# Kernel tuning notes

Hardware: AMD Instinct MI355X
Metric: run time of the kernel (lower is better)

## Reference

```python
import jax, jax.numpy as jnp
import numpy as np

B, S, H, NCOL, NH = 32, 512, 768, 32, 12
HD = H // NH  # head dim 64
LN_EPS = 1e-12


def setup_inputs() -> dict:
    key = jax.random.key(0)
    ks = jax.random.split(key, 20)
    s = 0.02
    inp = {
        'hidden_states': jax.random.normal(ks[0], (B, S, H), jnp.float32),
        'column_embeddings': jax.random.normal(ks[1], (B, NCOL, H), jnp.float32),
        'column_categories': jax.random.randint(ks[2], (B, NCOL), 0, 2, jnp.int32),
        'value_mask': jax.random.randint(ks[3], (B, S), 0, NCOL + 1, jnp.int32),
        'Wd': jax.random.normal(ks[4], (H, H), jnp.float32) * s,
        'bd': jnp.zeros((H,), jnp.float32),
        'Wc': jax.random.normal(ks[5], (H, H), jnp.float32) * s,
        'bc': jnp.zeros((H,), jnp.float32),
        'Wq': jax.random.normal(ks[6], (H, H), jnp.float32) * s,
        'bq': jnp.zeros((H,), jnp.float32),
        'Wk': jax.random.normal(ks[7], (H, H), jnp.float32) * s,
        'bk': jnp.zeros((H,), jnp.float32),
        'Wv': jax.random.normal(ks[8], (H, H), jnp.float32) * s,
        'bv': jnp.zeros((H,), jnp.float32),
        'Wo': jax.random.normal(ks[9], (H, H), jnp.float32) * s,
        'bo': jnp.zeros((H,), jnp.float32),
        'ln_g': jnp.ones((H,), jnp.float32),
        'ln_b': jnp.zeros((H,), jnp.float32),
    }
    return inp


def _layernorm(x, g, b):
    mu = jnp.mean(x, axis=-1, keepdims=True)
    var = jnp.mean(jnp.square(x - mu), axis=-1, keepdims=True)
    return (x - mu) * jax.lax.rsqrt(var + LN_EPS) * g + b


def reference(hidden_states, column_embeddings, column_categories, value_mask,
              Wd, bd, Wc, bc, Wq, bq, Wk, bk, Wv, bv, Wo, bo, ln_g, ln_b):
    # dense branch
    h_ = hidden_states @ Wd.T + bd  # [B,S,H]
    # column gather: zero out category==0 columns, prepend zero row for index 0
    table = column_embeddings * (column_categories == 1)[..., None].astype(column_embeddings.dtype)
    table = jnp.concatenate([jnp.zeros_like(table[:, :1]), table], axis=1)  # [B,NCOL+1,H]
    h_col = jnp.take_along_axis(table, value_mask[..., None].astype(jnp.int32), axis=1)  # [B,S,H]
    h = jax.nn.gelu(h_ + (h_col @ Wc.T + bc), approximate=False)
    # Roberta self-attention
    def heads(x):
        return x.reshape(B, S, NH, HD).transpose(0, 2, 1, 3)  # [B,NH,S,HD]
    q = heads(h @ Wq.T + bq)
    k = heads(h @ Wk.T + bk)
    v = heads(h @ Wv.T + bv)
    scores = jnp.einsum('bhsd,bhtd->bhst', q, k) / jnp.sqrt(jnp.float32(HD))
    probs = jax.nn.softmax(scores, axis=-1)
    ctx = jnp.einsum('bhst,bhtd->bhsd', probs, v).transpose(0, 2, 1, 3).reshape(B, S, H)
    # self-output: dense + residual + layernorm
    out = _layernorm(ctx @ Wo.T + bo + h, ln_g, ln_b)
    return out
```

## Files before the change

kernel.cpp:

```cpp
#include <hip/hip_runtime.h>
#include <hip/hip_bf16.h>
#include <math.h>
#include <stdint.h>

#define B_    32
#define S_    512
#define H_    768
#define NH_   12
#define HD_   64
#define NCOL_ 32
#define M_    (B_*S_)

typedef __bf16 bf16;
typedef __bf16 bf16x8 __attribute__((ext_vector_type(8)));
typedef __bf16 bf16x4 __attribute__((ext_vector_type(4)));
typedef float  f32x4  __attribute__((ext_vector_type(4)));

__device__ __forceinline__ void async_load16(const void* g, void* l) {
    __builtin_amdgcn_global_load_lds(
        (__attribute__((address_space(1))) unsigned int*)g,
        (__attribute__((address_space(3))) unsigned int*)l, 16, 0, 0);
}

__device__ __forceinline__ bf16x8 cvt8(const float* p) {
    const float4* fp = (const float4*)p;
    float4 x = fp[0], y = fp[1];
    bf16x8 r;
    r[0] = (bf16)x.x; r[1] = (bf16)x.y; r[2] = (bf16)x.z; r[3] = (bf16)x.w;
    r[4] = (bf16)y.x; r[5] = (bf16)y.y; r[6] = (bf16)y.z; r[7] = (bf16)y.w;
    return r;
}

__global__ __launch_bounds__(256) void cvt_kernel(
    const float* __restrict__ hidden, const float* __restrict__ ce,
    const int* __restrict__ cc, const int* __restrict__ vm,
    const float* __restrict__ Wd, const float* __restrict__ Wc,
    const float* __restrict__ Wq, const float* __restrict__ Wk,
    const float* __restrict__ Wv, const float* __restrict__ Wo,
    const float* __restrict__ bq, const float* __restrict__ bk,
    const float* __restrict__ bv,
    bf16* __restrict__ hbf, bf16* __restrict__ hcol,
    bf16* __restrict__ wpack, float* __restrict__ bqkv)
{
    int blk = blockIdx.x;
    if (blk < 6144) {
        int id = blk * 256 + threadIdx.x;
        int row = id / 96, c = id - row * 96;
        *(bf16x8*)&hbf[(long)row * H_ + c * 8] = cvt8(hidden + (long)row * H_ + c * 8);
    } else if (blk < 12288) {
        int id = (blk - 6144) * 256 + threadIdx.x;
        int row = id / 96, c = id - row * 96;
        int b = row >> 9;
        int m = vm[row];
        bf16x8 val;
#pragma unroll
        for (int i = 0; i < 8; i++) val[i] = (bf16)0.0f;
        if (m > 0) {
            int col = m - 1;
            if (cc[b * NCOL_ + col] == 1)
                val = cvt8(ce + ((long)(b * NCOL_ + col)) * H_ + c * 8);
        }
        *(bf16x8*)&hcol[(long)row * H_ + c * 8] = val;
    } else {
        int id = (blk - 12288) * 256 + threadIdx.x;
        if (id < 442368) {
            const float* src;
            int r = id;
            if      (r < 73728)  { src = Wd; }
            else if (r < 147456) { src = Wc; r -= 73728; }
            else if (r < 221184) { src = Wq; r -= 147456; }
            else if (r < 294912) { src = Wk; r -= 221184; }
            else if (r < 368640) { src = Wv; r -= 294912; }
            else                 { src = Wo; r -= 368640; }
            *(bf16x8*)&wpack[(long)id * 8] = cvt8(src + (long)r * 8);
        } else if (id < 442656) {
            int j0 = (id - 442368) * 8;
#pragma unroll
            for (int i = 0; i < 8; i++) {
                int j = j0 + i;
                float v = (j < 768) ? bq[j] : (j < 1536) ? bk[j - 768] : bv[j - 1536];
                bqkv[j] = v;
            }
        }
    }
}

template<int MODE>
__global__ __launch_bounds__(256, 3) void gemm_bt(
    const bf16* __restrict__ A0, const bf16* __restrict__ A1,
    const bf16* __restrict__ B0, const bf16* __restrict__ B1,
    const float* __restrict__ bias1, const float* __restrict__ bias2,
    const bf16* __restrict__ resid, bf16* __restrict__ out,
    int K, int KSPLIT)
{
    __shared__ __align__(16) bf16 SA[3][128 * 32];
    __shared__ __align__(16) bf16 SB[3][128 * 32];

    const int tid  = threadIdx.x;
    const int lane = tid & 63;
    const int wave = tid >> 6;
    const int wr   = wave >> 1;
    const int wc   = wave & 1;
    const int quad = lane >> 4;
    const int ln16 = lane & 15;
    const int m0   = blockIdx.x * 128;
    const int n0   = blockIdx.y * 128;

    int arow[2], acol[2];
#pragma unroll
    for (int q = 0; q < 2; q++) {
        int l = q * 256 + tid;
        int row = l >> 2;
        arow[q] = row;
        acol[q] = ((l & 3) ^ ((row >> 1) & 3)) * 8;
    }

    auto stage = [&](int kt, int bsel) {
        int kk = kt * 32;
        const bf16* ag = (kk < KSPLIT) ? A0 + kk : A1 + (kk - KSPLIT);
        const bf16* bg = (kk < KSPLIT) ? B0 + kk : B1 + (kk - KSPLIT);
        async_load16(ag + (long)(m0 + arow[0]) * H_ + acol[0], &SA[bsel][tid * 8]);
        async_load16(ag + (long)(m0 + arow[1]) * H_ + acol[1], &SA[bsel][2048 + tid * 8]);
        async_load16(bg + (long)(n0 + arow[0]) * H_ + acol[0], &SB[bsel][tid * 8]);
        async_load16(bg + (long)(n0 + arow[1]) * H_ + acol[1], &SB[bsel][2048 + tid * 8]);
    };

    f32x4 acc[4][4];
    const f32x4 zero4 = {0.f, 0.f, 0.f, 0.f};
#pragma unroll
    for (int i = 0; i < 4; i++)
#pragma unroll
        for (int j = 0; j < 4; j++) acc[i][j] = zero4;

    const int s4 = (ln16 >> 1) & 3;
    int aoff[4], boff[4];
#pragma unroll
    for (int i = 0; i < 4; i++) {
        aoff[i] = (wr * 64 + i * 16 + ln16) * 32 + (quad ^ s4) * 8;
        boff[i] = (wc * 64 + i * 16 + ln16) * 32 + (quad ^ s4) * 8;
    }

    const int nt = K >> 5;

    stage(0, 0);
    stage(1, 1);
    asm volatile("s_waitcnt vmcnt(4)" ::: "memory");
    __builtin_amdgcn_sched_barrier(0);
    __builtin_amdgcn_s_barrier();

    int bs = 0;
    for (int t = 0; t < nt; ++t) {
        const int ps = (bs + 2 >= 3) ? bs - 1 : bs + 2;

        bf16x8 af[4], bfr[4];
#pragma unroll
        for (int i = 0; i < 4; i++) af[i]  = *(const bf16x8*)&SA[bs][aoff[i]];
#pragma unroll
        for (int j = 0; j < 4; j++) bfr[j] = *(const bf16x8*)&SB[bs][boff[j]];
        if (t + 2 < nt) stage(t + 2, ps);

        __builtin_amdgcn_s_setprio(1);
#pragma unroll
        for (int i = 0; i < 4; i++)
#pragma unroll
            for (int j = 0; j < 4; j++)
                acc[i][j] = __builtin_amdgcn_mfma_f32_16x16x32_bf16(af[i], bfr[j], acc[i][j], 0, 0, 0);
        __builtin_amdgcn_s_setprio(0);

        if (t + 2 < nt)       { asm volatile("s_waitcnt vmcnt(4)" ::: "memory"); }
        else if (t + 1 < nt)  { asm volatile("s_waitcnt vmcnt(0)" ::: "memory"); }
        __builtin_amdgcn_sched_barrier(0);
        if (t + 1 < nt) __builtin_amdgcn_s_barrier();
        bs = (bs + 1 == 3) ? 0 : bs + 1;
    }

    const int c_r = quad * 4;
    const int c_c = ln16;

    int sec = 0;
    if (MODE == 1) sec = (n0 >= 1536) ? 2 : ((n0 >= 768) ? 1 : 0);
    bf16* dst = (MODE == 1) ? out + (long)sec * M_ * H_ : out;

#pragma unroll
    for (int j = 0; j < 4; j++) {
        const int col = n0 + wc * 64 + j * 16 + c_c;
        float bias = bias1[col];
        if (MODE == 0) bias += bias2[col];
#pragma unroll
        for (int i = 0; i < 4; i++) {
            if (MODE == 1 && sec == 2) {
                const int row0 = m0 + wr * 64 + i * 16 + c_r;
                int b = row0 >> 9, s = row0 & 511;
                int cs = col - 1536;
                int head = cs >> 6, d = cs & 63;
                bf16x4 pk;
#pragma unroll
                for (int r = 0; r < 4; r++) pk[r] = (bf16)(acc[i][j][r] + bias);
                *(bf16x4*)&dst[(((long)(b * NH_ + head)) * HD_ + d) * S_ + s] = pk;
            } else {
#pragma unroll
                for (int r = 0; r < 4; r++) {
                    const int row = m0 + wr * 64 + i * 16 + c_r + r;
                    float v = acc[i][j][r] + bias;
                    if (MODE == 0) {
                        v = 0.5f * v * (1.0f + erff(v * 0.70710678118654752f));
                        dst[(long)row * H_ + col] = (bf16)v;
                    } else if (MODE == 1) {
                        int b = row >> 9, s = row & 511;
                        int cs = col - sec * 768;
                        int head = cs >> 6, d = cs & 63;
                        dst[(((long)(b * NH_ + head)) * S_ + s) * HD_ + d] = (bf16)v;
                    } else {
                        v += (float)resid[(long)row * H_ + col];
                        dst[(long)row * H_ + col] = (bf16)v;
                    }
                }
            }
        }
    }
}

#define QP 72

__global__ __launch_bounds__(256) void attn_kernel(
    const bf16* __restrict__ q, const bf16* __restrict__ k,
    const bf16* __restrict__ vt, bf16* __restrict__ ctx)
{
    __shared__ __align__(16) bf16 Qs[64 * QP];
    __shared__ __align__(16) bf16 Ks[64 * QP];
    __shared__ __align__(16) bf16 Vt[64 * QP];
    __shared__ __align__(16) bf16 Ps[4][16 * QP];

    const int tid  = threadIdx.x;
    const int lane = tid & 63;
    const int w    = tid >> 6;
    const int quad = lane >> 4;
    const int ln16 = lane & 15;

    const int bid = blockIdx.x;
    const int qt  = bid / 384;
    const int g   = bid - qt * 384;
    const int b   = g / 12;
    const int h   = g - b * 12;
    const long base = ((long)(b * NH_ + h)) * S_ * HD_;

    const int r0 = tid >> 2;
    const int e0 = (tid & 3) * 16;

    {
        const bf16* qg = q + base + (long)qt * 64 * HD_;
        *(uint4*)&Qs[r0 * QP + e0]     = *(const uint4*)&qg[r0 * HD_ + e0];
        *(uint4*)&Qs[r0 * QP + e0 + 8] = *(const uint4*)&qg[r0 * HD_ + e0 + 8];
    }
    const bf16* kg = k  + base;
    const bf16* vg = vt + base;
    uint4 kr0 = *(const uint4*)&kg[r0 * HD_ + e0];
    uint4 kr1 = *(const uint4*)&kg[r0 * HD_ + e0 + 8];
    uint4 vr0 = *(const uint4*)&vg[(long)r0 * S_ + e0];
    uint4 vr1 = *(const uint4*)&vg[(long)r0 * S_ + e0 + 8];
    __syncthreads();

    const bf16x8 bq0 = *(const bf16x8*)&Qs[(w * 16 + ln16) * QP + quad * 8];
    const bf16x8 bq1 = *(const bf16x8*)&Qs[(w * 16 + ln16) * QP + 32 + quad * 8];

    f32x4 O[4];
    const f32x4 zero4 = {0.f, 0.f, 0.f, 0.f};
#pragma unroll
    for (int t = 0; t < 4; t++) O[t] = zero4;
    float mo = -1e30f, l = 0.f;

    for (int kc = 0; kc < 8; kc++) {
        __syncthreads();
        *(uint4*)&Ks[r0 * QP + e0]     = kr0;
        *(uint4*)&Ks[r0 * QP + e0 + 8] = kr1;
        *(uint4*)&Vt[r0 * QP + e0]     = vr0;
        *(uint4*)&Vt[r0 * QP + e0 + 8] = vr1;
        {
            int kcn = (kc < 7) ? kc + 1 : 7;
            kr0 = *(const uint4*)&kg[(long)kcn * 64 * HD_ + r0 * HD_ + e0];
            kr1 = *(const uint4*)&kg[(long)kcn * 64 * HD_ + r0 * HD_ + e0 + 8];
            vr0 = *(const uint4*)&vg[(long)r0 * S_ + kcn * 64 + e0];
            vr1 = *(const uint4*)&vg[(long)r0 * S_ + kcn * 64 + e0 + 8];
        }
        __syncthreads();

        f32x4 sc[4];
#pragma unroll
        for (int i = 0; i < 4; i++) {
            bf16x8 a0 = *(const bf16x8*)&Ks[(i * 16 + ln16) * QP + quad * 8];
            bf16x8 a1 = *(const bf16x8*)&Ks[(i * 16 + ln16) * QP + 32 + quad * 8];
            sc[i] = zero4;
            sc[i] = __builtin_amdgcn_mfma_f32_16x16x32_bf16(a0, bq0, sc[i], 0, 0, 0);
            sc[i] = __builtin_amdgcn_mfma_f32_16x16x32_bf16(a1, bq1, sc[i], 0, 0, 0);
        }

        float cm = -1e30f;
#pragma unroll
        for (int i = 0; i < 4; i++)
#pragma unroll
            for (int r = 0; r < 4; r++) {
                float s = sc[i][r] * 0.125f;
                sc[i][r] = s;
                cm = fmaxf(cm, s);
            }
        cm = fmaxf(cm, __shfl_xor(cm, 16));
        cm = fmaxf(cm, __shfl_xor(cm, 32));
        float mn = fmaxf(mo, cm);
        float alpha = __expf(mo - mn);
        float rs = 0.f;
#pragma unroll
        for (int i = 0; i < 4; i++) {
            bf16x4 pk;
#pragma unroll
            for (int r = 0; r < 4; r++) {
                float p = __expf(sc[i][r] - mn);
                rs += p;
                pk[r] = (bf16)p;
            }
            *(bf16x4*)&Ps[w][ln16 * QP + i * 16 + quad * 4] = pk;
        }
        rs += __shfl_xor(rs, 16);
        rs += __shfl_xor(rs, 32);
        l  = l * alpha + rs;
        mo = mn;
#pragma unroll
        for (int t = 0; t < 4; t++)
#pragma unroll
            for (int r = 0; r < 4; r++) O[t][r] *= alpha;

        bf16x8 bp0 = *(const bf16x8*)&Ps[w][ln16 * QP + quad * 8];
        bf16x8 bp1 = *(const bf16x8*)&Ps[w][ln16 * QP + 32 + quad * 8];
#pragma unroll
        for (int dt = 0; dt < 4; dt++) {
            bf16x8 a0 = *(const bf16x8*)&Vt[(dt * 16 + ln16) * QP + quad * 8];
            bf16x8 a1 = *(const bf16x8*)&Vt[(dt * 16 + ln16) * QP + 32 + quad * 8];
            O[dt] = __builtin_amdgcn_mfma_f32_16x16x32_bf16(a0, bp0, O[dt], 0, 0, 0);
            O[dt] = __builtin_amdgcn_mfma_f32_16x16x32_bf16(a1, bp1, O[dt], 0, 0, 0);
        }
    }

    {
        float inv = 1.0f / l;
#pragma unroll
        for (int dt = 0; dt < 4; dt++) {
            bf16x4 ov;
#pragma unroll
            for (int r = 0; r < 4; r++) ov[r] = (bf16)(O[dt][r] * inv);
            *(bf16x4*)&Qs[(w * 16 + ln16) * QP + dt * 16 + quad * 4] = ov;
        }
    }
    __syncthreads();
    {
        uint4 o0 = *(const uint4*)&Qs[r0 * QP + e0];
        uint4 o1 = *(const uint4*)&Qs[r0 * QP + e0 + 8];
        bf16* cg = ctx + ((long)(b * S_ + qt * 64 + r0)) * H_ + h * HD_;
        *(uint4*)&cg[e0]     = o0;
        *(uint4*)&cg[e0 + 8] = o1;
    }
}

__global__ __launch_bounds__(256) void ln_kernel(
    const bf16* __restrict__ y, const float* __restrict__ g,
    const float* __restrict__ be, float* __restrict__ out)
{
    const int lane = threadIdx.x & 63;
    const int w    = threadIdx.x >> 6;
    const long row = (long)blockIdx.x * 4 + w;
    const bf16* yr = y + row * H_;

    float x[12];
    float sum = 0.f, ss = 0.f;
#pragma unroll
    for (int j = 0; j < 12; j++) {
        x[j] = (float)yr[j * 64 + lane];
        sum += x[j];
        ss  += x[j] * x[j];
    }
#pragma unroll
    for (int m = 1; m < 64; m <<= 1) {
        sum += __shfl_xor(sum, m);
        ss  += __shfl_xor(ss, m);
    }
    const float mu  = sum * (1.0f / 768.0f);
    float var = ss * (1.0f / 768.0f) - mu * mu;
    const float rs = rsqrtf(fmaxf(var, 0.f) + 1e-12f);
#pragma unroll
    for (int j = 0; j < 12; j++) {
        int c = j * 64 + lane;
        out[row * H_ + c] = (x[j] - mu) * rs * g[c] + be[c];
    }
}

extern "C" void kernel_launch(void* const* d_in, const int* in_sizes, int n_in,
                              void* d_out, int out_size, void* d_ws, size_t ws_size,
                              hipStream_t stream)
{
    const float* hidden = (const float*)d_in[0];
    const float* ce     = (const float*)d_in[1];
    const int*   cc     = (const int*)d_in[2];
    const int*   vm     = (const int*)d_in[3];
    const float* Wd     = (const float*)d_in[4];
    const float* bd     = (const float*)d_in[5];
    const float* Wc     = (const float*)d_in[6];
    const float* bc     = (const float*)d_in[7];
    const float* Wq     = (const float*)d_in[8];
    const float* bq     = (const float*)d_in[9];
    const float* Wk     = (const float*)d_in[10];
    const float* bk     = (const float*)d_in[11];
    const float* Wv     = (const float*)d_in[12];
    const float* bv     = (const float*)d_in[13];
    const float* Wo     = (const float*)d_in[14];
    const float* bo     = (const float*)d_in[15];
    const float* lng    = (const float*)d_in[16];
    const float* lnb    = (const float*)d_in[17];

    const long NE = (long)M_ * H_;
    bf16* ws   = (bf16*)d_ws;
    bf16* hbuf = ws;
    bf16* qkv  = ws + NE;
    bf16* hbf  = qkv;
    bf16* hcol = qkv + NE;
    bf16* qb   = qkv;
    bf16* kb   = qkv + NE;
    bf16* vb   = qkv + 2 * NE;
    bf16* wpack = ws + 4 * NE;
    const bf16* Wd_b  = wpack;
    const bf16* Wc_b  = wpack + 589824;
    const bf16* Wq_b  = wpack + 1179648;
    const bf16* Wk_b  = wpack + 1769472;
    const bf16* Wv_b  = wpack + 2359296;
    const bf16* Wo_b  = wpack + 2949120;
    float* bqkv = (float*)(wpack + 3538944);
    bf16* ctx = (bf16*)d_out;

    cvt_kernel<<<14018, 256, 0, stream>>>(hidden, ce, cc, vm, Wd, Wc, Wq, Wk, Wv, Wo,
                                          bq, bk, bv, hbf, hcol, wpack, bqkv);

    dim3 g6(M_ / 128, 6);
    dim3 g18(M_ / 128, 18);
    gemm_bt<0><<<g6, 256, 0, stream>>>(hbf, hcol, Wd_b, Wc_b, bd, bc, nullptr, hbuf, 2 * H_, H_);
    gemm_bt<1><<<g18, 256, 0, stream>>>(hbuf, hbuf, Wq_b, Wq_b, bqkv, nullptr, nullptr, qkv, H_, 3 * H_);
    attn_kernel<<<3072, 256, 0, stream>>>(qb, kb, vb, ctx);
    gemm_bt<2><<<g6, 256, 0, stream>>>(ctx, ctx, Wo_b, Wo_b, bo, nullptr, hbuf, hbuf, H_, H_);
    ln_kernel<<<M_ / 4, 256, 0, stream>>>(hbuf, lng, lnb, (float*)d_out);
}
```

Before: 370.8 us.

## Add dedicated QKV GEMM with 256-row tiles and LDS-staged coalesced head-layout stores

Replaces the generic MODE 1 GEMM for the QKV projection with a dedicated kernel. It uses 512-thread blocks covering 256x128 output tiles with triple-buffered async LDS loads. The epilogue stages each wave's 64x64 result in LDS (transposed for V) so it can issue 16-byte coalesced stores into the per-head Q/K layout and the transposed V layout. The old path wrote scattered 2-byte or 8-byte elements. The larger tile halves the reloads of B per output, but it uses more LDS and registers per block, which may reduce occupancy.

```diff
diff --git a/kernel.cpp b/kernel.cpp
--- a/kernel.cpp
+++ b/kernel.cpp
@@ -85,6 +85,141 @@
     }
 }
 
+__global__ __launch_bounds__(512, 4) void gemm_qkv(
+    const bf16* __restrict__ A, const bf16* __restrict__ Bw,
+    const float* __restrict__ bias, bf16* __restrict__ out)
+{
+    __shared__ __align__(16) bf16 LB[36864];
+
+    const int tid  = threadIdx.x;
+    const int lane = tid & 63;
+    const int wave = tid >> 6;
+    const int wr   = wave >> 1;
+    const int wc   = wave & 1;
+    const int quad = lane >> 4;
+    const int ln16 = lane & 15;
+    const int m0   = blockIdx.x * 256;
+    const int n0   = blockIdx.y * 128;
+
+    int arow[2], acol[2];
+#pragma unroll
+    for (int q = 0; q < 2; q++) {
+        int l = q * 512 + tid;
+        int row = l >> 2;
+        arow[q] = row;
+        acol[q] = ((l & 3) ^ ((row >> 1) & 3)) * 8;
+    }
+    const int brow = tid >> 2;
+    const int bcol = ((tid & 3) ^ ((brow >> 1) & 3)) * 8;
+
+    auto stage = [&](int kt, int bsel) {
+        int kk = kt * 32;
+        const bf16* ag = A + kk;
+        const bf16* bg = Bw + kk;
+        bf16* SAb = &LB[bsel * 8192];
+        bf16* SBb = &LB[24576 + bsel * 4096];
+        async_load16(ag + (long)(m0 + arow[0]) * H_ + acol[0], SAb + tid * 8);
+        async_load16(ag + (long)(m0 + arow[1]) * H_ + acol[1], SAb + 4096 + tid * 8);
+        async_load16(bg + (long)(n0 + brow)    * H_ + bcol,    SBb + tid * 8);
+    };
+
+    f32x4 acc[4][4];
+    const f32x4 zero4 = {0.f, 0.f, 0.f, 0.f};
+#pragma unroll
+    for (int i = 0; i < 4; i++)
+#pragma unroll
+        for (int j = 0; j < 4; j++) acc[i][j] = zero4;
+
+    const int s4 = (ln16 >> 1) & 3;
+    int aoff[4], boff[4];
+#pragma unroll
+    for (int i = 0; i < 4; i++) {
+        aoff[i] = (wr * 64 + i * 16 + ln16) * 32 + (quad ^ s4) * 8;
+        boff[i] = (wc * 64 + i * 16 + ln16) * 32 + (quad ^ s4) * 8;
+    }
+
+    const int nt = 24;
+
+    stage(0, 0);
+    stage(1, 1);
+    asm volatile("s_waitcnt vmcnt(3)" ::: "memory");
+    __builtin_amdgcn_sched_barrier(0);
+    __builtin_amdgcn_s_barrier();
+
+    int bs = 0;
+    for (int t = 0; t < nt; ++t) {
+        const int ps = (bs + 2 >= 3) ? bs - 1 : bs + 2;
+
+        bf16x8 af[4], bfr[4];
+#pragma unroll
+        for (int i = 0; i < 4; i++) af[i]  = *(const bf16x8*)&LB[bs * 8192 + aoff[i]];
+#pragma unroll
+        for (int j = 0; j < 4; j++) bfr[j] = *(const bf16x8*)&LB[24576 + bs * 4096 + boff[j]];
+        if (t + 2 < nt) stage(t + 2, ps);
+
+        __builtin_amdgcn_s_setprio(1);
+#pragma unroll
+        for (int i = 0; i < 4; i++)
+#pragma unroll
+            for (int j = 0; j < 4; j++)
+                acc[i][j] = __builtin_amdgcn_mfma_f32_16x16x32_bf16(af[i], bfr[j], acc[i][j], 0, 0, 0);
+        __builtin_amdgcn_s_setprio(0);
+
+        if (t + 2 < nt)       { asm volatile("s_waitcnt vmcnt(3)" ::: "memory"); }
+        else if (t + 1 < nt)  { asm volatile("s_waitcnt vmcnt(0)" ::: "memory"); }
+        __builtin_amdgcn_sched_barrier(0);
+        if (t + 1 < nt) __builtin_amdgcn_s_barrier();
+        bs = (bs + 1 == 3) ? 0 : bs + 1;
+    }
+
+    __syncthreads();
+    bf16* scr = &LB[wave * 4608];
+
+    const int cs0  = n0 + wc * 64;
+    const int sec  = (cs0 >= 1536) ? 2 : ((cs0 >= 768) ? 1 : 0);
+    const int head = (cs0 - sec * 768) >> 6;
+    bf16* dst = out + (long)sec * M_ * H_;
+
+#pragma unroll
+    for (int j = 0; j < 4; j++) {
+        const int d_loc = j * 16 + ln16;
+        const float bj = bias[cs0 + d_loc];
+#pragma unroll
+        for (int i = 0; i < 4; i++) {
+#pragma unroll
+            for (int r = 0; r < 4; r++) {
+                const int s_loc = i * 16 + quad * 4 + r;
+                const float v = acc[i][j][r] + bj;
+                scr[(sec == 2) ? (d_loc * 72 + s_loc) : (s_loc * 72 + d_loc)] = (bf16)v;
+            }
+        }
+    }
+    asm volatile("s_waitcnt lgkmcnt(0)" ::: "memory");
+    __builtin_amdgcn_sched_barrier(0);
+
+    const int g8 = lane >> 3;
+    const int o8 = (lane & 7) * 8;
+    if (sec < 2) {
+#pragma unroll
+        for (int it = 0; it < 8; it++) {
+            const int s_loc = it * 8 + g8;
+            const int row_s = m0 + wr * 64 + s_loc;
+            const int b = row_s >> 9, s = row_s & 511;
+            *(bf16x8*)&dst[(((long)(b * NH_ + head)) * S_ + s) * HD_ + o8] =
+                *(const bf16x8*)&scr[s_loc * 72 + o8];
+        }
+    } else {
+        const int row0 = m0 + wr * 64;
+        const int b = row0 >> 9, sb = row0 & 511;
+#pragma unroll
+        for (int it = 0; it < 8; it++) {
+            const int d_loc = it * 8 + g8;
+            *(bf16x8*)&dst[(((long)(b * NH_ + head)) * HD_ + d_loc) * S_ + sb + o8] =
+                *(const bf16x8*)&scr[d_loc * 72 + o8];
+        }
+    }
+}
+
 template<int MODE>
 __global__ __launch_bounds__(256, 3) void gemm_bt(
     const bf16* __restrict__ A0, const bf16* __restrict__ A1,
@@ -177,10 +312,6 @@
     const int c_r = quad * 4;
     const int c_c = ln16;
 
-    int sec = 0;
-    if (MODE == 1) sec = (n0 >= 1536) ? 2 : ((n0 >= 768) ? 1 : 0);
-    bf16* dst = (MODE == 1) ? out + (long)sec * M_ * H_ : out;
-
 #pragma unroll
     for (int j = 0; j < 4; j++) {
         const int col = n0 + wc * 64 + j * 16 + c_c;
@@ -188,32 +319,16 @@
         if (MODE == 0) bias += bias2[col];
 #pragma unroll
         for (int i = 0; i < 4; i++) {
-            if (MODE == 1 && sec == 2) {
-                const int row0 = m0 + wr * 64 + i * 16 + c_r;
-                int b = row0 >> 9, s = row0 & 511;
-                int cs = col - 1536;
-                int head = cs >> 6, d = cs & 63;
-                bf16x4 pk;
-#pragma unroll
-                for (int r = 0; r < 4; r++) pk[r] = (bf16)(acc[i][j][r] + bias);
-                *(bf16x4*)&dst[(((long)(b * NH_ + head)) * HD_ + d) * S_ + s] = pk;
-            } else {
-#pragma unroll
-                for (int r = 0; r < 4; r++) {
-                    const int row = m0 + wr * 64 + i * 16 + c_r + r;
-                    float v = acc[i][j][r] + bias;
-                    if (MODE == 0) {
-                        v = 0.5f * v * (1.0f + erff(v * 0.70710678118654752f));
-                        dst[(long)row * H_ + col] = (bf16)v;
-                    } else if (MODE == 1) {
-                        int b = row >> 9, s = row & 511;
-                        int cs = col - sec * 768;
-                        int head = cs >> 6, d = cs & 63;
-                        dst[(((long)(b * NH_ + head)) * S_ + s) * HD_ + d] = (bf16)v;
-                    } else {
-                        v += (float)resid[(long)row * H_ + col];
-                        dst[(long)row * H_ + col] = (bf16)v;
-                    }
+#pragma unroll
+            for (int r = 0; r < 4; r++) {
+                const int row = m0 + wr * 64 + i * 16 + c_r + r;
+                float v = acc[i][j][r] + bias;
+                if (MODE == 0) {
+                    v = 0.5f * v * (1.0f + erff(v * 0.70710678118654752f));
+                    out[(long)row * H_ + col] = (bf16)v;
+                } else {
+                    v += (float)resid[(long)row * H_ + col];
+                    out[(long)row * H_ + col] = (bf16)v;
                 }
             }
         }
@@ -427,8 +542,6 @@
     const bf16* Wd_b  = wpack;
     const bf16* Wc_b  = wpack + 589824;
     const bf16* Wq_b  = wpack + 1179648;
-    const bf16* Wk_b  = wpack + 1769472;
-    const bf16* Wv_b  = wpack + 2359296;
     const bf16* Wo_b  = wpack + 2949120;
     float* bqkv = (float*)(wpack + 3538944);
     bf16* ctx = (bf16*)d_out;
@@ -437,9 +550,8 @@
                                           bq, bk, bv, hbf, hcol, wpack, bqkv);
 
     dim3 g6(M_ / 128, 6);
-    dim3 g18(M_ / 128, 18);
     gemm_bt<0><<<g6, 256, 0, stream>>>(hbf, hcol, Wd_b, Wc_b, bd, bc, nullptr, hbuf, 2 * H_, H_);
-    gemm_bt<1><<<g18, 256, 0, stream>>>(hbuf, hbuf, Wq_b, Wq_b, bqkv, nullptr, nullptr, qkv, H_, 3 * H_);
+    gemm_qkv<<<dim3(M_ / 256, 18), 512, 0, stream>>>(hbuf, Wq_b, bqkv, qkv);
     attn_kernel<<<3072, 256, 0, stream>>>(qb, kb, vb, ctx);
     gemm_bt<2><<<g6, 256, 0, stream>>>(ctx, ctx, Wo_b, Wo_b, bo, nullptr, hbuf, hbuf, H_, H_);
     ln_kernel<<<M_ / 4, 256, 0, stream>>>(hbuf, lng, lnb, (float*)d_out);
```

After: 366.7 us, median of 2. About the same (-1.1%).
